# Optimization experiments

Hardware: AMD Instinct MI355X
Metric: run time of the kernel (lower is better)

Reference implementation:

```python
import jax, jax.numpy as jnp
import numpy as np

BATCH, SEQ = 4, 2048
D_MODEL, INNER, STATE, K, FFN = 384, 768, 16, 4, 1024


def setup_inputs() -> dict:
    key = jax.random.key(0)
    ks = jax.random.split(key, 12)
    def g(k, shape, scale=0.02):
        return jax.random.normal(k, shape, jnp.float32) * scale
    return {
        "x": jax.random.normal(ks[0], (BATCH, SEQ, D_MODEL), jnp.float32),
        "rms1_w": jnp.ones((D_MODEL,), jnp.float32),
        "rms2_w": jnp.ones((D_MODEL,), jnp.float32),
        "in_proj_w": g(ks[1], (D_MODEL, 2 * INNER)),
        "conv_w": g(ks[2], (K, INNER, INNER)),
        "conv_b": jnp.zeros((INNER,), jnp.float32),
        "x_proj_w": g(ks[3], (INNER, 2 * STATE)),
        "dt_proj_w": g(ks[4], (INNER, INNER)),
        "dt_proj_b": jnp.zeros((INNER,), jnp.float32),
        "A_log": jnp.log(jax.random.uniform(ks[5], (INNER, STATE), jnp.float32, 1.0, 16.0)),
        "D_param": jnp.ones((INNER,), jnp.float32),
        "out_proj_w": g(ks[6], (INNER, D_MODEL)),
        "ln_gamma": jnp.ones((D_MODEL,), jnp.float32),
        "ln_beta": jnp.zeros((D_MODEL,), jnp.float32),
        "gate_w": g(ks[7], (D_MODEL, FFN)),
        "up_w": g(ks[8], (D_MODEL, FFN)),
        "down_w": g(ks[9], (FFN, D_MODEL)),
    }


def rms_norm(x, w, eps=1e-6):
    norm = jnp.sqrt(jnp.mean(jnp.square(x), axis=-1, keepdims=True) + eps)
    return x / norm * w


def layer_norm(x, gamma, beta, eps=1e-5):
    mu = jnp.mean(x, axis=-1, keepdims=True)
    var = jnp.mean(jnp.square(x - mu), axis=-1, keepdims=True)
    return (x - mu) / jnp.sqrt(var + eps) * gamma + beta


def selective_scan(x, delta, A_log, Bm, Cm, Dp):
    # x, delta: [B,L,Di]; Bm, Cm: [B,L,N]; A_log: [Di,N]; Dp: [Di]
    delta = jax.nn.softplus(delta)
    A = -jnp.exp(A_log)                          # [Di,N]
    A_disc = jnp.exp(delta[..., None] * A)       # [B,L,Di,N]
    B_disc = delta[..., None] * Bm[:, :, None, :]  # [B,L,Di,N]
    xs = jnp.moveaxis(x, 1, 0)       # [L,B,Di]
    As = jnp.moveaxis(A_disc, 1, 0)  # [L,B,Di,N]
    Bs = jnp.moveaxis(B_disc, 1, 0)  # [L,B,Di,N]
    Cs = jnp.moveaxis(Cm, 1, 0)      # [L,B,N]
    h0 = jnp.zeros((x.shape[0], A_log.shape[0], A_log.shape[1]), x.dtype)
    def step(h, inp):
        x_t, A_t, B_t, C_t = inp
        h = A_t * h + B_t * x_t[..., None]          # [B,Di,N]
        y_t = jnp.einsum('bdn,bn->bd', h, C_t)      # [B,Di]
        return h, y_t
    _, ys = jax.lax.scan(step, h0, (xs, As, Bs, Cs))
    y = jnp.moveaxis(ys, 0, 1)       # [B,L,Di]
    return y + Dp * x


def mamba_core(h, in_proj_w, conv_w, conv_b, x_proj_w, dt_proj_w, dt_proj_b,
               A_log, D_param, out_proj_w, ln_gamma, ln_beta):
    xz = h @ in_proj_w                             # [B,L,2*Di]
    x_inner, z = jnp.split(xz, 2, axis=-1)
    # Conv1D SAME padding (k=4 -> pad (1,2)), channels-last, kernel [W,I,O]
    x_conv = jax.lax.conv_general_dilated(
        x_inner, conv_w, window_strides=(1,), padding='SAME',
        dimension_numbers=('NWC', 'WIO', 'NWC')) + conv_b
    x_conv = jax.nn.silu(x_conv)
    Bm, Cm = jnp.split(x_conv @ x_proj_w, 2, axis=-1)  # each [B,L,N]
    delta = x_conv @ dt_proj_w + dt_proj_b            # [B,L,Di]
    y = selective_scan(x_conv, delta, A_log, Bm, Cm, D_param)
    y = y * jax.nn.silu(z)
    out = y @ out_proj_w
    return layer_norm(out, ln_gamma, ln_beta)


def reference(x, rms1_w, rms2_w, in_proj_w, conv_w, conv_b, x_proj_w,
              dt_proj_w, dt_proj_b, A_log, D_param, out_proj_w, ln_gamma,
              ln_beta, gate_w, up_w, down_w):
    residual = x
    h = rms_norm(x, rms1_w)
    h = mamba_core(h, in_proj_w, conv_w, conv_b, x_proj_w, dt_proj_w,
                   dt_proj_b, A_log, D_param, out_proj_w, ln_gamma, ln_beta)
    x = residual + h  # dropout inactive (training=False)
    residual = x
    h = rms_norm(x, rms2_w)
    hidden = jax.nn.silu(h @ gate_w) * (h @ up_w)
    x = residual + hidden @ down_w
    return x
```

## Files before the change

kernel.cpp:

```cpp
#include <hip/hip_runtime.h>
#include <hip/hip_bf16.h>


using u16 = unsigned short;
using u32 = unsigned int;
using short8 = __attribute__((ext_vector_type(8))) short;
using f32x4  = __attribute__((ext_vector_type(4))) float;

#define TTOK 8192
#define DM 384
#define DI 768
#define NST 16
#define LSEQ 2048
#define NCH 64
#define LCH 32

#define SWZ_R(row, quad) \
  ((row) * 32 + ((((quad) ^ (row) ^ ((row) >> 2)) & 3) * 8))
#define SWZ_W(tid) SWZ_R((tid) >> 2, (tid) & 3)

__device__ __forceinline__ float bf2f(u16 a) {
  u32 u = ((u32)a) << 16;
  float f; __builtin_memcpy(&f, &u, 4); return f;
}
__device__ __forceinline__ u16 f2bf(float f) {
  u32 u; __builtin_memcpy(&u, &f, 4);
  u32 r = (u + 0x7fffu + ((u >> 16) & 1u)) >> 16;
  return (u16)r;
}
__device__ __forceinline__ int probe_bf(const void* rw) {
  return (((const u32*)rw)[0] == 0x3F803F80u) ? 1 : 0;
}
__device__ __forceinline__ float ld_in(const void* p, int i, int isbf) {
  return isbf ? bf2f(((const u16*)p)[i]) : ((const float*)p)[i];
}
__device__ __forceinline__ float fexp2(float x) {
#if __has_builtin(__builtin_amdgcn_exp2f)
  return __builtin_amdgcn_exp2f(x);
#else
  return exp2f(x);
#endif
}
__device__ __forceinline__ float wave_sum(float v) {
#pragma unroll
  for (int off = 32; off > 0; off >>= 1) v += __shfl_xor(v, off, 64);
  return v;
}

__device__ __forceinline__ void gl_lds16(const u16* g, u16* l) {
  __builtin_amdgcn_global_load_lds(
      (const __attribute__((address_space(1))) u32*)g,
      (__attribute__((address_space(3))) u32*)l, 16, 0, 0);
}

#define V_CB 0
#define V_DB 768
#define V_DP 1536
#define V_R1 2304
#define V_R2 2688
#define V_GA 3072
#define V_BE 3456

__global__ __launch_bounds__(256) void k_prep(
    const void* __restrict__ x, const void* __restrict__ in_proj,
    const void* __restrict__ conv_w, const void* __restrict__ dt_w,
    const void* __restrict__ x_proj, const void* __restrict__ out_proj,
    const void* __restrict__ gate_w, const void* __restrict__ up_w,
    const void* __restrict__ down_w, const void* __restrict__ A_log,
    const void* __restrict__ conv_b, const void* __restrict__ dt_b,
    const void* __restrict__ Dp, const void* __restrict__ rms1_w,
    const void* __restrict__ rms2_w, const void* __restrict__ gamma,
    const void* __restrict__ beta,
    u16* __restrict__ W1T, u16* __restrict__ WCT, u16* __restrict__ W45T,
    u16* __restrict__ W5T, u16* __restrict__ W6T, u16* __restrict__ W7T,
    float* __restrict__ An2T, u16* __restrict__ vecs,
    u16* __restrict__ WinX, u16* __restrict__ h1pad) {
  const int isbf = probe_bf(rms1_w);
  const int bx = blockIdx.x;
  const int tid = threadIdx.x;
  __shared__ u16 lt[64 * 66];

  if (bx < 1236) {
    const void* src; size_t soff = 0; u16* dst; int R, C, tpr, lo;
    if (bx < 144)       { src = in_proj;  dst = W1T;  R = 384;  C = 1536; tpr = 24; lo = bx; }
    else if (bx < 720)  { int tp = (bx - 144) / 144; lo = (bx - 144) % 144;
                          src = conv_w; soff = (size_t)tp * 589824;
                          dst = WCT + (size_t)tp * 589824; R = 768; C = 768; tpr = 12; }
    else if (bx < 864)  { src = dt_w;     dst = W45T; R = 768;  C = 768;  tpr = 12; lo = bx - 720; }
    else if (bx < 876)  { src = x_proj;   dst = W45T + (size_t)768 * 768;
                          R = 768; C = 32; tpr = 1; lo = bx - 864; }
    else if (bx < 948)  { src = out_proj; dst = W5T;  R = 768;  C = 384;  tpr = 6;  lo = bx - 876; }
    else if (bx < 1044) { src = gate_w;   dst = W6T;  R = 384;  C = 1024; tpr = 16; lo = bx - 948; }
    else if (bx < 1140) { src = up_w;     dst = W6T + (size_t)1024 * 384;
                          R = 384; C = 1024; tpr = 16; lo = bx - 1044; }
    else                { src = down_w;   dst = W7T;  R = 1024; C = 384;  tpr = 6;  lo = bx - 1140; }
    int tr = lo / tpr, tc = lo % tpr;
    int r0 = tr * 64, c0 = tc * 64;
#pragma unroll
    for (int i = 0; i < 16; ++i) {
      int el = i * 256 + tid, lr = el >> 6, lc = el & 63;
      if (c0 + lc < C)
        lt[lr * 66 + lc] =
            f2bf(ld_in(src, (int)(soff + (size_t)(r0 + lr) * C + c0 + lc), isbf));
    }
    __syncthreads();
#pragma unroll
    for (int i = 0; i < 16; ++i) {
      int el = i * 256 + tid, orow = el >> 6, oc = el & 63;
      if (c0 + orow < C)
        dst[(size_t)(c0 + orow) * R + r0 + oc] = lt[oc * 66 + orow];
    }
    return;
  }
  if (bx < 5332) {
    int half = tid >> 7;
    int t = (bx - 1236) * 2 + half;
    int tid2 = tid & 127;
    int lane = tid & 63, wv = tid >> 6;
    float v[3]; float q = 0.f;
#pragma unroll
    for (int j = 0; j < 3; ++j) {
      v[j] = ld_in(x, t * DM + tid2 + j * 128, isbf);
      q += v[j] * v[j];
    }
    q = wave_sum(q);
    float* rq = (float*)lt;
    if (lane == 0) rq[wv] = q;
    __syncthreads();
    float rr = rsqrtf((rq[half * 2] + rq[half * 2 + 1]) * (1.f / DM) + 1e-6f);
    int b = t >> 11, l = t & 2047;
    size_t orow = ((size_t)(b * 2051 + l + 1)) * DM;
#pragma unroll
    for (int j = 0; j < 3; ++j) {
      int i = tid2 + j * 128;
      h1pad[orow + i] = f2bf(v[j] * rr * ld_in(rms1_w, i, isbf));
    }
    return;
  }
  if (bx < 6484) {
    int lo = (bx - 5332) * 256 + tid;
    int i = lo / 768, j = lo % 768;
    WinX[lo] = f2bf(ld_in(in_proj, i * 1536 + j, isbf));
    return;
  }
  if (bx < 6532) {
    int lo = (bx - 6484) * 256 + tid;
    if (lo < 12288) {
      int d = lo >> 4, n = lo & 15;
      An2T[n * DI + d] = -__expf(ld_in(A_log, lo, isbf)) * 1.44269504f;
    }
    return;
  }
  if (bx < 6547) {
    int lo = (bx - 6532) * 256 + tid;
    if (lo < 3840) {
      const void* s; int o;
      if      (lo < 768)  { s = conv_b; o = lo; }
      else if (lo < 1536) { s = dt_b;   o = lo - 768; }
      else if (lo < 2304) { s = Dp;     o = lo - 1536; }
      else if (lo < 2688) { s = rms1_w; o = lo - 2304; }
      else if (lo < 3072) { s = rms2_w; o = lo - 2688; }
      else if (lo < 3456) { s = gamma;  o = lo - 3072; }
      else                { s = beta;   o = lo - 3456; }
      vecs[lo] = f2bf(ld_in(s, o, isbf));
    }
    return;
  }
  {
    int lo = (bx - 6547) * 256 + tid;
    if (lo < 4608) {
      int b = lo / (3 * DM), rem = lo % (3 * DM);
      int which = rem / DM, i = rem % DM;
      int row = b * 2051 + (which == 0 ? 0 : (2048 + which));
      h1pad[(size_t)row * DM + i] = 0;
    }
  }
}

__global__ __launch_bounds__(128) void k_lnrms(const float* __restrict__ outm,
                                               const void* __restrict__ xin,
                                               const void* __restrict__ rw,
                                               const u16* __restrict__ vecs,
                                               float* __restrict__ x2f,
                                               u16* __restrict__ h2) {
  const int isbf = probe_bf(rw);
  int t = blockIdx.x, tid = threadIdx.x;
  int lane = tid & 63, wid = tid >> 6;
  float v[3]; float s = 0.f, q = 0.f;
#pragma unroll
  for (int j = 0; j < 3; ++j) {
    v[j] = outm[(size_t)t * DM + tid + j * 128];
    s += v[j]; q += v[j] * v[j];
  }
  s = wave_sum(s); q = wave_sum(q);
  __shared__ float rs[2], rq[2], r2[2];
  if (lane == 0) { rs[wid] = s; rq[wid] = q; }
  __syncthreads();
  float mu = (rs[0] + rs[1]) * (1.f / DM);
  float var = (rq[0] + rq[1]) * (1.f / DM) - mu * mu;
  float rstd = rsqrtf(var + 1e-5f);
  float x2v[3]; float q2 = 0.f;
#pragma unroll
  for (int j = 0; j < 3; ++j) {
    int i = tid + j * 128;
    float ln = (v[j] - mu) * rstd * bf2f(vecs[V_GA + i]) + bf2f(vecs[V_BE + i]);
    x2v[j] = ld_in(xin, t * DM + i, isbf) + ln;
    x2f[(size_t)t * DM + i] = x2v[j];
    q2 += x2v[j] * x2v[j];
  }
  q2 = wave_sum(q2);
  if (lane == 0) r2[wid] = q2;
  __syncthreads();
  float rr = rsqrtf((r2[0] + r2[1]) * (1.f / DM) + 1e-6f);
#pragma unroll
  for (int j = 0; j < 3; ++j) {
    int i = tid + j * 128;
    h2[(size_t)t * DM + i] = f2bf(x2v[j] * rr * bf2f(vecs[V_R2 + i]));
  }
}

template <int EPI, int KDIM>
__global__ __launch_bounds__(256) void gemm_bt(
    const u16* __restrict__ A, const u16* __restrict__ BT,
    float* __restrict__ o1, u16* __restrict__ ob1,
    const float* __restrict__ res, const void* __restrict__ fl) {
  __shared__ u16 smem[2][8192];
  const int tid = threadIdx.x;
  const int lane = tid & 63, wid = tid >> 6;
  const int wm = (wid >> 1) << 5, wn = (wid & 1) << 5;
  const int fr = lane & 15, quad = lane >> 4;
  const int m0 = blockIdx.x * 64, n0 = blockIdx.y * 64;

  f32x4 acc[2][2] = {};

  const int wrow = (wid << 4) | (lane >> 2);
  const int sq = ((lane & 3) ^ wrow ^ (wrow >> 2)) & 3;
  const u16* BTe = (EPI == 6) ? BT + (size_t)blockIdx.z * 589824 : BT;
  const u16* srcA = A + (size_t)(m0 + wrow) * KDIM + sq * 8;
  const u16* srcB = BTe + (size_t)(n0 + wrow) * KDIM + sq * 8;
  u16* lw = &smem[0][0] + (wid << 9);

  auto stage = [&](int buf, int kt) {
    u16* lb = lw + buf * 8192;
    gl_lds16(srcA + kt,      lb);
    gl_lds16(srcA + kt + 32, lb + 2048);
    gl_lds16(srcB + kt,      lb + 4096);
    gl_lds16(srcB + kt + 32, lb + 6144);
  };

  stage(0, 0);
  int cur = 0;

#pragma unroll 1
  for (int kt = 0; kt < KDIM; kt += 64) {
    __syncthreads();
    if (kt + 64 < KDIM) stage(cur ^ 1, kt + 64);
    const u16* sm = &smem[cur][0];
#pragma unroll
    for (int kh = 0; kh < 2; ++kh) {
      const int ao = kh * 2048, bo = 4096 + kh * 2048;
      short8 af[2], bfg[2];
#pragma unroll
      for (int i = 0; i < 2; ++i)
        af[i] = *(const short8*)&sm[ao + SWZ_R(wm + i * 16 + fr, quad)];
#pragma unroll
      for (int i = 0; i < 2; ++i)
        bfg[i] = *(const short8*)&sm[bo + SWZ_R(wn + i * 16 + fr, quad)];
#pragma unroll
      for (int mt = 0; mt < 2; ++mt)
#pragma unroll
        for (int nt = 0; nt < 2; ++nt)
          acc[mt][nt] = __builtin_amdgcn_mfma_f32_16x16x32_bf16(
              af[mt], bfg[nt], acc[mt][nt], 0, 0, 0);
    }
    cur ^= 1;
  }

  int isbf = 0;
  if (EPI == 5) isbf = probe_bf(fl);

#pragma unroll
  for (int mt = 0; mt < 2; ++mt) {
#pragma unroll
    for (int nt = 0; nt < 2; ++nt) {
#pragma unroll
      for (int r = 0; r < 4; ++r) {
        int t = m0 + wm + mt * 16 + quad * 4 + r;
        int n = n0 + wn + nt * 16 + fr;
        float v = acc[mt][nt][r];
        if (EPI == 3) {
          o1[(size_t)t * DM + n] = v;
        } else if (EPI == 5) {
          float val = v + res[(size_t)t * DM + n];
          if (isbf) ob1[(size_t)t * DM + n] = f2bf(val);
          else      o1[(size_t)t * DM + n] = val;
        } else if (EPI == 6) {
          ob1[(size_t)n * 1536 + blockIdx.z * 384 + t] = f2bf(v);
        }
      }
    }
  }
}

__global__ __launch_bounds__(256) void gemm2_128(
    const u16* __restrict__ A, const u16* __restrict__ BT,
    float* __restrict__ o2, u16* __restrict__ ob1,
    const u16* __restrict__ bias) {
  constexpr int KDIM = 768;
  __shared__ u16 smem[2][12288];
  const int tid = threadIdx.x;
  const int lane = tid & 63, wid = tid >> 6;
  const int wm = (wid >> 1) << 6, wn = (wid & 1) << 5;
  const int fr = lane & 15, quad = lane >> 4;
  const int m0 = blockIdx.x * 128, n0 = blockIdx.y * 64;

  f32x4 acc[4][2] = {};

  const int ra = (wid << 5) | (lane >> 2);
  const int sqa = ((lane & 3) ^ ra ^ (ra >> 2)) & 3;
  const int rb = (wid << 4) | (lane >> 2);
  const int sqb = ((lane & 3) ^ rb ^ (rb >> 2)) & 3;
  const u16* srcA = A + (size_t)(m0 + ra) * KDIM + sqa * 8;
  const u16* srcB = BT + (size_t)(n0 + rb) * KDIM + sqb * 8;
  u16* lA = &smem[0][0] + (wid << 10);
  u16* lB = &smem[0][8192] + (wid << 9);

  auto stage = [&](int buf, int kt) {
    u16* a = lA + buf * 12288;
    u16* b = lB + buf * 12288;
    gl_lds16(srcA + kt,                           a);
    gl_lds16(srcA + kt + (size_t)16 * KDIM,       a + 512);
    gl_lds16(srcA + kt + 32,                      a + 4096);
    gl_lds16(srcA + kt + 32 + (size_t)16 * KDIM,  a + 4608);
    gl_lds16(srcB + kt,       b);
    gl_lds16(srcB + kt + 32,  b + 2048);
  };

  stage(0, 0);
  int cur = 0;

#pragma unroll 1
  for (int kt = 0; kt < KDIM; kt += 64) {
    __syncthreads();
    if (kt + 64 < KDIM) stage(cur ^ 1, kt + 64);
    const u16* sm = &smem[cur][0];
#pragma unroll
    for (int kh = 0; kh < 2; ++kh) {
      const int ao = kh * 4096, bo = 8192 + kh * 2048;
      short8 af[4], bfg[2];
#pragma unroll
      for (int i = 0; i < 4; ++i)
        af[i] = *(const short8*)&sm[ao + SWZ_R(wm + i * 16 + fr, quad)];
#pragma unroll
      for (int i = 0; i < 2; ++i)
        bfg[i] = *(const short8*)&sm[bo + SWZ_R(wn + i * 16 + fr, quad)];
#pragma unroll
      for (int mt = 0; mt < 4; ++mt)
#pragma unroll
        for (int nt = 0; nt < 2; ++nt)
          acc[mt][nt] = __builtin_amdgcn_mfma_f32_16x16x32_bf16(
              af[mt], bfg[nt], acc[mt][nt], 0, 0, 0);
    }
    cur ^= 1;
  }

#pragma unroll
  for (int nt = 0; nt < 2; ++nt) {
    const int n = n0 + wn + nt * 16 + fr;
    if (n < DI) {
      const float bv = bf2f(bias[n]);
#pragma unroll
      for (int mt = 0; mt < 4; ++mt) {
#pragma unroll
        for (int r = 0; r < 4; ++r) {
          int t = m0 + wm + mt * 16 + quad * 4 + r;
          float xx = acc[mt][nt][r] + bv;
          float e = fexp2(xx * 1.44269504f);
          float sp = (xx > 20.f) ? xx : 0.69314718056f * __log2f(1.f + e);
          ob1[(size_t)t * DI + n] = f2bf(sp);
        }
      }
    } else if (n < DI + 32) {
#pragma unroll
      for (int mt = 0; mt < 4; ++mt) {
#pragma unroll
        for (int r = 0; r < 4; ++r) {
          int t = m0 + wm + mt * 16 + quad * 4 + r;
          o2[(size_t)t * 32 + (n - DI)] = acc[mt][nt][r];
        }
      }
    }
  }
}

__global__ __launch_bounds__(256) void gemm_xz(
    const u16* __restrict__ A, const u16* __restrict__ WC,
    const u16* __restrict__ WZ, u16* __restrict__ xconv,
    u16* __restrict__ zbuf, const u16* __restrict__ bias) {
  __shared__ u16 smem[12288];
  const int tid = threadIdx.x;
  const int lane = tid & 63, wid = tid >> 6;
  const int wm = (wid >> 1) << 6, wn = (wid & 1) << 5;
  const int fr = lane & 15, quad = lane >> 4;
  const int yb = blockIdx.y;
  const bool isz = yb >= 12;
  const int kd = isz ? 384 : 1536;
  const u16* BT = isz ? WZ : WC;
  const int kldb = isz ? 384 : 1536;
  const int n0 = (isz ? yb - 12 : yb) * 64;
  const int m0 = blockIdx.x * 128;

  f32x4 acc[4][2] = {};

  const int ra = (wid << 5) | (lane >> 2);
  const int sqa = ((lane & 3) ^ ra ^ (ra >> 2)) & 3;
  const int rb = (wid << 4) | (lane >> 2);
  const int sqb = ((lane & 3) ^ rb ^ (rb >> 2)) & 3;
  const u16* srcB = BT + (size_t)(n0 + rb) * kldb + sqb * 8;
  const int b = m0 >> 11, l0 = m0 & 2047;
  const u16* srcA0 =
      A + (size_t)(b * 2051 + l0 + ra + (isz ? 1 : 0)) * DM + sqa * 8;
  u16* lA = &smem[0] + (wid << 10);
  u16* lB = &smem[8192] + (wid << 9);

  int wc = 0, ic = 0;
  auto stage = [&](int kt) {
    const u16* sa = srcA0 + (size_t)wc * DM + ic;
    gl_lds16(sa,                         lA);
    gl_lds16(sa + (size_t)16 * DM,       lA + 512);
    gl_lds16(sa + 32,                    lA + 4096);
    gl_lds16(sa + 32 + (size_t)16 * DM,  lA + 4608);
    gl_lds16(srcB + kt,       lB);
    gl_lds16(srcB + kt + 32,  lB + 2048);
    ic += 64; if (ic == 384) { ic = 0; ++wc; }
  };

#pragma unroll 1
  for (int kt = 0; kt < kd; kt += 64) {
    __syncthreads();
    stage(kt);
    __syncthreads();
#pragma unroll
    for (int kh = 0; kh < 2; ++kh) {
      const int ao = kh * 4096, bo = 8192 + kh * 2048;
      short8 af[4], bfg[2];
#pragma unroll
      for (int i = 0; i < 4; ++i)
        af[i] = *(const short8*)&smem[ao + SWZ_R(wm + i * 16 + fr, quad)];
#pragma unroll
      for (int i = 0; i < 2; ++i)
        bfg[i] = *(const short8*)&smem[bo + SWZ_R(wn + i * 16 + fr, quad)];
#pragma unroll
      for (int mt = 0; mt < 4; ++mt)
#pragma unroll
        for (int nt = 0; nt < 2; ++nt)
          acc[mt][nt] = __builtin_amdgcn_mfma_f32_16x16x32_bf16(
              af[mt], bfg[nt], acc[mt][nt], 0, 0, 0);
    }
  }

#pragma unroll
  for (int mt = 0; mt < 4; ++mt) {
#pragma unroll
    for (int nt = 0; nt < 2; ++nt) {
#pragma unroll
      for (int r = 0; r < 4; ++r) {
        int t = m0 + wm + mt * 16 + quad * 4 + r;
        int n = n0 + wn + nt * 16 + fr;
        float v = acc[mt][nt][r];
        if (isz) {
          zbuf[(size_t)t * DI + n] = f2bf(v);
        } else {
          float xx = v + bf2f(bias[n]);
          float sg = 1.f / (1.f + __expf(-xx));
          xconv[(size_t)t * DI + n] = f2bf(xx * sg);
        }
      }
    }
  }
}

__global__ __launch_bounds__(256) void gemm_gu(
    const u16* __restrict__ A, const u16* __restrict__ W6T,
    u16* __restrict__ hid) {
  __shared__ u16 smem[16384];
  const int tid = threadIdx.x;
  const int lane = tid & 63, wid = tid >> 6;
  const int wm = (wid >> 1) << 6, wn = (wid & 1) << 5;
  const int fr = lane & 15, quad = lane >> 4;
  const int m0 = blockIdx.x * 128, n0 = blockIdx.y * 64;

  f32x4 accg[4][2] = {}, accu[4][2] = {};

  const int ra = (wid << 5) | (lane >> 2);
  const int sqa = ((lane & 3) ^ ra ^ (ra >> 2)) & 3;
  const int rb = (wid << 4) | (lane >> 2);
  const int sqb = ((lane & 3) ^ rb ^ (rb >> 2)) & 3;
  const u16* srcA = A + (size_t)(m0 + ra) * DM + sqa * 8;
  const u16* srcG = W6T + (size_t)(n0 + rb) * DM + sqb * 8;
  const u16* srcU = W6T + (size_t)(1024 + n0 + rb) * DM + sqb * 8;
  u16* lA = &smem[0] + (wid << 10);
  u16* lG = &smem[8192] + (wid << 9);
  u16* lU = &smem[12288] + (wid << 9);

  auto stage = [&](int kt) {
    gl_lds16(srcA + kt,                        lA);
    gl_lds16(srcA + kt + (size_t)16 * DM,      lA + 512);
    gl_lds16(srcA + kt + 32,                   lA + 4096);
    gl_lds16(srcA + kt + 32 + (size_t)16 * DM, lA + 4608);
    gl_lds16(srcG + kt,       lG);
    gl_lds16(srcG + kt + 32,  lG + 2048);
    gl_lds16(srcU + kt,       lU);
    gl_lds16(srcU + kt + 32,  lU + 2048);
  };

#pragma unroll 1
  for (int kt = 0; kt < DM; kt += 64) {
    __syncthreads();
    stage(kt);
    __syncthreads();
#pragma unroll
    for (int kh = 0; kh < 2; ++kh) {
      const int ao = kh * 4096, go = 8192 + kh * 2048, uo = 12288 + kh * 2048;
      short8 af[4], bg[2], bu[2];
#pragma unroll
      for (int i = 0; i < 4; ++i)
        af[i] = *(const short8*)&smem[ao + SWZ_R(wm + i * 16 + fr, quad)];
#pragma unroll
      for (int i = 0; i < 2; ++i) {
        bg[i] = *(const short8*)&smem[go + SWZ_R(wn + i * 16 + fr, quad)];
        bu[i] = *(const short8*)&smem[uo + SWZ_R(wn + i * 16 + fr, quad)];
      }
#pragma unroll
      for (int mt = 0; mt < 4; ++mt)
#pragma unroll
        for (int nt = 0; nt < 2; ++nt) {
          accg[mt][nt] = __builtin_amdgcn_mfma_f32_16x16x32_bf16(
              af[mt], bg[nt], accg[mt][nt], 0, 0, 0);
          accu[mt][nt] = __builtin_amdgcn_mfma_f32_16x16x32_bf16(
              af[mt], bu[nt], accu[mt][nt], 0, 0, 0);
        }
    }
  }

#pragma unroll
  for (int mt = 0; mt < 4; ++mt) {
#pragma unroll
    for (int nt = 0; nt < 2; ++nt) {
#pragma unroll
      for (int r = 0; r < 4; ++r) {
        int t = m0 + wm + mt * 16 + quad * 4 + r;
        int n = n0 + wn + nt * 16 + fr;
        float g = accg[mt][nt][r];
        float u = accu[mt][nt][r];
        float sg = 1.f / (1.f + __expf(-g));
        hid[(size_t)t * 1024 + n] = f2bf(g * sg * u);
      }
    }
  }
}

__global__ __launch_bounds__(256) void k_scan1(
    const u16* __restrict__ deltab, const u16* __restrict__ xconv,
    const float* __restrict__ BC, const float* __restrict__ An2T,
    float* __restrict__ hlb, float* __restrict__ Pb) {
  __shared__ float bcs[LCH * 32];
  int gid = blockIdx.x * 256 + threadIdx.x;
  int d = gid % DI, bc = gid / DI, c = bc & (NCH - 1), b = bc >> 6;
  int row0 = b * LSEQ + c * LCH;
  ((float4*)bcs)[threadIdx.x] =
      ((const float4*)(BC + (size_t)row0 * 32))[threadIdx.x];
  float An[NST];
#pragma unroll
  for (int n = 0; n < NST; ++n) An[n] = An2T[n * DI + d];
  float h[NST], P[NST];
#pragma unroll
  for (int n = 0; n < NST; ++n) { h[n] = 0.f; P[n] = 1.f; }
  float dt = bf2f(deltab[(size_t)row0 * DI + d]);
  float xv = bf2f(xconv[(size_t)row0 * DI + d]);
  __syncthreads();
  for (int s = 0; s < LCH; ++s) {
    float dtc = dt, xvc = xv;
    if (s + 1 < LCH) {
      int r2 = row0 + s + 1;
      dt = bf2f(deltab[(size_t)r2 * DI + d]);
      xv = bf2f(xconv[(size_t)r2 * DI + d]);
    }
    const float4* br = (const float4*)&bcs[s * 32];
    float4 q0 = br[0], q1 = br[1], q2 = br[2], q3 = br[3];
    float Bm[NST] = {q0.x, q0.y, q0.z, q0.w, q1.x, q1.y, q1.z, q1.w,
                     q2.x, q2.y, q2.z, q2.w, q3.x, q3.y, q3.z, q3.w};
    float dxv = dtc * xvc;
#pragma unroll
    for (int n = 0; n < NST; ++n) {
      float a = fexp2(dtc * An[n]);
      h[n] = fmaf(a, h[n], dxv * Bm[n]);
      P[n] *= a;
    }
  }
  float4* ph = (float4*)(hlb + (size_t)gid * NST);
  float4* pp = (float4*)(Pb + (size_t)gid * NST);
#pragma unroll
  for (int i = 0; i < 4; ++i) {
    ph[i] = make_float4(h[4*i], h[4*i+1], h[4*i+2], h[4*i+3]);
    pp[i] = make_float4(P[4*i], P[4*i+1], P[4*i+2], P[4*i+3]);
  }
}

__global__ __launch_bounds__(256) void k_scan2(const float* __restrict__ hlb,
                                               const float* __restrict__ Pb,
                                               float* __restrict__ hin) {
  int gid = blockIdx.x * 256 + threadIdx.x;
  int n = gid & 15, bd = gid >> 4;
  int d = bd % DI, b = bd / DI;
  size_t base = ((size_t)(b * NCH) * DI + d) * NST + n;
  const size_t cstride = (size_t)DI * NST;
  float H = 0.f;
  float hc = hlb[base], pc = Pb[base];
  for (int c = 0; c < NCH; ++c) {
    size_t idx = base + (size_t)c * cstride;
    float hn = 0.f, pn = 0.f;
    if (c + 1 < NCH) { hn = hlb[idx + cstride]; pn = Pb[idx + cstride]; }
    hin[idx] = H;
    H = hc + pc * H;
    hc = hn; pc = pn;
  }
}

__global__ __launch_bounds__(256) void k_scan3(
    const u16* __restrict__ deltab, const u16* __restrict__ xconv,
    const float* __restrict__ BC, const float* __restrict__ An2T,
    const float* __restrict__ hinb, const u16* __restrict__ zb,
    const u16* __restrict__ vecs, u16* __restrict__ ys) {
  __shared__ float bcs[LCH * 32];
  int gid = blockIdx.x * 256 + threadIdx.x;
  int d = gid % DI, bc = gid / DI, c = bc & (NCH - 1), b = bc >> 6;
  int row0 = b * LSEQ + c * LCH;
  ((float4*)bcs)[threadIdx.x] =
      ((const float4*)(BC + (size_t)row0 * 32))[threadIdx.x];
  float An[NST];
#pragma unroll
  for (int n = 0; n < NST; ++n) An[n] = An2T[n * DI + d];
  float h[NST];
  {
    const float4* hp = (const float4*)(hinb + (size_t)gid * NST);
#pragma unroll
    for (int i = 0; i < 4; ++i) {
      float4 t = hp[i];
      h[4*i] = t.x; h[4*i+1] = t.y; h[4*i+2] = t.z; h[4*i+3] = t.w;
    }
  }
  float Dd = bf2f(vecs[V_DP + d]);
  float dt = bf2f(deltab[(size_t)row0 * DI + d]);
  float xv = bf2f(xconv[(size_t)row0 * DI + d]);
  float zv = bf2f(zb[(size_t)row0 * DI + d]);
  __syncthreads();
  for (int s = 0; s < LCH; ++s) {
    int row = row0 + s;
    float dtc = dt, xvc = xv, zvc = zv;
    if (s + 1 < LCH) {
      int r2 = row + 1;
      dt = bf2f(deltab[(size_t)r2 * DI + d]);
      xv = bf2f(xconv[(size_t)r2 * DI + d]);
      zv = bf2f(zb[(size_t)r2 * DI + d]);
    }
    const float4* br = (const float4*)&bcs[s * 32];
    float4 q0 = br[0], q1 = br[1], q2 = br[2], q3 = br[3];
    float4 c0 = br[4], c1 = br[5], c2 = br[6], c3 = br[7];
    float Bm[NST] = {q0.x, q0.y, q0.z, q0.w, q1.x, q1.y, q1.z, q1.w,
                     q2.x, q2.y, q2.z, q2.w, q3.x, q3.y, q3.z, q3.w};
    float Cm[NST] = {c0.x, c0.y, c0.z, c0.w, c1.x, c1.y, c1.z, c1.w,
                     c2.x, c2.y, c2.z, c2.w, c3.x, c3.y, c3.z, c3.w};
    float dxv = dtc * xvc;
    float yp[4] = {0.f, 0.f, 0.f, 0.f};
#pragma unroll
    for (int n = 0; n < NST; ++n) {
      float a = fexp2(dtc * An[n]);
      h[n] = fmaf(a, h[n], dxv * Bm[n]);
      yp[n & 3] = fmaf(h[n], Cm[n], yp[n & 3]);
    }
    float y = (yp[0] + yp[1]) + (yp[2] + yp[3]);
    float sz = zvc / (1.f + __expf(-zvc));
    ys[(size_t)row * DI + d] = f2bf((y + Dd * xvc) * sz);
  }
}

extern "C" void kernel_launch(void* const* d_in, const int* in_sizes, int n_in,
                              void* d_out, int out_size, void* d_ws,
                              size_t ws_size, hipStream_t stream) {
  (void)in_sizes; (void)n_in; (void)out_size;
  const void* x        = d_in[0];
  const void* rms1_w   = d_in[1];
  const void* rms2_w   = d_in[2];
  const void* in_proj  = d_in[3];
  const void* conv_w   = d_in[4];
  const void* conv_b   = d_in[5];
  const void* x_proj   = d_in[6];
  const void* dt_w     = d_in[7];
  const void* dt_b     = d_in[8];
  const void* A_log    = d_in[9];
  const void* Dp       = d_in[10];
  const void* out_proj = d_in[11];
  const void* gamma    = d_in[12];
  const void* beta     = d_in[13];
  const void* gate_w   = d_in[14];
  const void* up_w     = d_in[15];
  const void* down_w   = d_in[16];

  char* ws = (char*)d_ws;
  size_t off = 0;
  auto alloc = [&](size_t bytes) -> void* {
    void* p = ws + off;
    off = (off + bytes + 255) & ~(size_t)255;
    return p;
  };
  u16*   W1T   = (u16*)alloc((size_t)1536 * 384 * 2);
  u16*   WCT   = (u16*)alloc((size_t)4 * 768 * 768 * 2);
  u16*   W45T  = (u16*)alloc((size_t)896 * 768 * 2);
  u16*   W5T   = (u16*)alloc((size_t)384 * 768 * 2);
  u16*   W6T   = (u16*)alloc((size_t)2048 * 384 * 2);
  u16*   W7T   = (u16*)alloc((size_t)384 * 1024 * 2);
  float* An2T  = (float*)alloc((size_t)16 * 768 * 4);
  u16*   vecs  = (u16*)alloc(3840 * 2);
  u16*   WinX  = (u16*)alloc((size_t)384 * 768 * 2);
  u16*   WcombT= (u16*)alloc((size_t)768 * 1536 * 2);
  u16*   h1pad = (u16*)alloc((size_t)4 * 2051 * 384 * 2);
  u16*   zbuf  = (u16*)alloc((size_t)8192 * 768 * 2);
  u16*   xconv = (u16*)alloc((size_t)8192 * 768 * 2);
  u16*   deltab= (u16*)alloc((size_t)8192 * 768 * 2);
  float* BCb   = (float*)alloc((size_t)8192 * 32 * 4);
  float* hl    = (float*)alloc((size_t)196608 * 16 * 4);
  float* Pb    = (float*)alloc((size_t)196608 * 16 * 4);
  float* hin   = (float*)alloc((size_t)196608 * 16 * 4);
  u16*   ys   = (u16*)hl;
  float* outm = Pb;
  float* x2f  = hin;
  u16*   h2   = h1pad;
  u16*   hid  = (u16*)hl;

  if (off > ws_size) return;

  k_prep<<<6565, 256, 0, stream>>>(
      x, in_proj, conv_w, dt_w, x_proj, out_proj, gate_w, up_w, down_w,
      A_log, conv_b, dt_b, Dp, rms1_w, rms2_w, gamma, beta,
      W1T, WCT, W45T, W5T, W6T, W7T, An2T, vecs, WinX, h1pad);

  gemm_bt<6, 768><<<dim3(6, 12, 4), 256, 0, stream>>>(
      WinX, WCT, nullptr, WcombT, nullptr, nullptr);

  gemm_xz<<<dim3(64, 24), 256, 0, stream>>>(
      h1pad, WcombT, W1T + (size_t)768 * 384, xconv, zbuf, vecs + V_CB);

  gemm2_128<<<dim3(64, 13), 256, 0, stream>>>(
      xconv, W45T, BCb, deltab, vecs + V_DB);

  k_scan1<<<768, 256, 0, stream>>>(deltab, xconv, BCb, An2T, hl, Pb);
  k_scan2<<<192, 256, 0, stream>>>(hl, Pb, hin);
  k_scan3<<<768, 256, 0, stream>>>(deltab, xconv, BCb, An2T, hin, zbuf, vecs,
                                   ys);

  gemm_bt<3, 768><<<dim3(128, 6), 256, 0, stream>>>(
      ys, W5T, outm, nullptr, nullptr, nullptr);
  k_lnrms<<<8192, 128, 0, stream>>>(outm, x, rms1_w, vecs, x2f, h2);

  gemm_gu<<<dim3(64, 16), 256, 0, stream>>>(h2, W6T, hid);
  gemm_bt<5, 1024><<<dim3(128, 6), 256, 0, stream>>>(
      hid, W7T, (float*)d_out, (u16*)d_out, x2f, rms1_w);
}
```

Measured before the change: 305.4 us.

## Double-buffer gemm_xz LDS and replace per-state chunk decay products with delta sums

gemm_xz now uses two LDS buffers and prefetches the next k-tile while computing the current one, which removes one barrier per iteration. This mirrors the gemm_bt pipeline and doubles the kernel's shared memory. The chunked scan no longer accumulates and stores a per-state decay product P. Scan1 stores only the sum of delta per chunk and channel, and scan2 rebuilds P as exp2(An*S), which cuts the writes and reads of a large float buffer at the cost of one exp per step. The rebuilt P can differ slightly in rounding from the old running product.

```diff
diff --git a/kernel.cpp b/kernel.cpp
--- a/kernel.cpp
+++ b/kernel.cpp
@@ -327,13 +327,13 @@
 
   auto stage = [&](int buf, int kt) {
     u16* a = lA + buf * 12288;
-    u16* b = lB + buf * 12288;
+    u16* bb = lB + buf * 12288;
     gl_lds16(srcA + kt,                           a);
     gl_lds16(srcA + kt + (size_t)16 * KDIM,       a + 512);
     gl_lds16(srcA + kt + 32,                      a + 4096);
     gl_lds16(srcA + kt + 32 + (size_t)16 * KDIM,  a + 4608);
-    gl_lds16(srcB + kt,       b);
-    gl_lds16(srcB + kt + 32,  b + 2048);
+    gl_lds16(srcB + kt,       bb);
+    gl_lds16(srcB + kt + 32,  bb + 2048);
   };
 
   stage(0, 0);
@@ -397,7 +397,7 @@
     const u16* __restrict__ A, const u16* __restrict__ WC,
     const u16* __restrict__ WZ, u16* __restrict__ xconv,
     u16* __restrict__ zbuf, const u16* __restrict__ bias) {
-  __shared__ u16 smem[12288];
+  __shared__ u16 smem[2][12288];
   const int tid = threadIdx.x;
   const int lane = tid & 63, wid = tid >> 6;
   const int wm = (wid >> 1) << 6, wn = (wid & 1) << 5;
@@ -420,36 +420,41 @@
   const int b = m0 >> 11, l0 = m0 & 2047;
   const u16* srcA0 =
       A + (size_t)(b * 2051 + l0 + ra + (isz ? 1 : 0)) * DM + sqa * 8;
-  u16* lA = &smem[0] + (wid << 10);
-  u16* lB = &smem[8192] + (wid << 9);
+  u16* lA = &smem[0][0] + (wid << 10);
+  u16* lB = &smem[0][8192] + (wid << 9);
 
   int wc = 0, ic = 0;
-  auto stage = [&](int kt) {
+  auto stage = [&](int buf, int kt) {
     const u16* sa = srcA0 + (size_t)wc * DM + ic;
-    gl_lds16(sa,                         lA);
-    gl_lds16(sa + (size_t)16 * DM,       lA + 512);
-    gl_lds16(sa + 32,                    lA + 4096);
-    gl_lds16(sa + 32 + (size_t)16 * DM,  lA + 4608);
-    gl_lds16(srcB + kt,       lB);
-    gl_lds16(srcB + kt + 32,  lB + 2048);
+    u16* a = lA + buf * 12288;
+    u16* bb = lB + buf * 12288;
+    gl_lds16(sa,                         a);
+    gl_lds16(sa + (size_t)16 * DM,       a + 512);
+    gl_lds16(sa + 32,                    a + 4096);
+    gl_lds16(sa + 32 + (size_t)16 * DM,  a + 4608);
+    gl_lds16(srcB + kt,       bb);
+    gl_lds16(srcB + kt + 32,  bb + 2048);
     ic += 64; if (ic == 384) { ic = 0; ++wc; }
   };
+
+  stage(0, 0);
+  int cur = 0;
 
 #pragma unroll 1
   for (int kt = 0; kt < kd; kt += 64) {
     __syncthreads();
-    stage(kt);
-    __syncthreads();
+    if (kt + 64 < kd) stage(cur ^ 1, kt + 64);
+    const u16* sm = &smem[cur][0];
 #pragma unroll
     for (int kh = 0; kh < 2; ++kh) {
       const int ao = kh * 4096, bo = 8192 + kh * 2048;
       short8 af[4], bfg[2];
 #pragma unroll
       for (int i = 0; i < 4; ++i)
-        af[i] = *(const short8*)&smem[ao + SWZ_R(wm + i * 16 + fr, quad)];
+        af[i] = *(const short8*)&sm[ao + SWZ_R(wm + i * 16 + fr, quad)];
 #pragma unroll
       for (int i = 0; i < 2; ++i)
-        bfg[i] = *(const short8*)&smem[bo + SWZ_R(wn + i * 16 + fr, quad)];
+        bfg[i] = *(const short8*)&sm[bo + SWZ_R(wn + i * 16 + fr, quad)];
 #pragma unroll
       for (int mt = 0; mt < 4; ++mt)
 #pragma unroll
@@ -457,6 +462,7 @@
           acc[mt][nt] = __builtin_amdgcn_mfma_f32_16x16x32_bf16(
               af[mt], bfg[nt], acc[mt][nt], 0, 0, 0);
     }
+    cur ^= 1;
   }
 
 #pragma unroll
@@ -563,7 +569,7 @@
 __global__ __launch_bounds__(256) void k_scan1(
     const u16* __restrict__ deltab, const u16* __restrict__ xconv,
     const float* __restrict__ BC, const float* __restrict__ An2T,
-    float* __restrict__ hlb, float* __restrict__ Pb) {
+    float* __restrict__ hlb, float* __restrict__ Sb) {
   __shared__ float bcs[LCH * 32];
   int gid = blockIdx.x * 256 + threadIdx.x;
   int d = gid % DI, bc = gid / DI, c = bc & (NCH - 1), b = bc >> 6;
@@ -573,9 +579,10 @@
   float An[NST];
 #pragma unroll
   for (int n = 0; n < NST; ++n) An[n] = An2T[n * DI + d];
-  float h[NST], P[NST];
-#pragma unroll
-  for (int n = 0; n < NST; ++n) { h[n] = 0.f; P[n] = 1.f; }
+  float h[NST];
+#pragma unroll
+  for (int n = 0; n < NST; ++n) h[n] = 0.f;
+  float S = 0.f;
   float dt = bf2f(deltab[(size_t)row0 * DI + d]);
   float xv = bf2f(xconv[(size_t)row0 * DI + d]);
   __syncthreads();
@@ -591,39 +598,37 @@
     float Bm[NST] = {q0.x, q0.y, q0.z, q0.w, q1.x, q1.y, q1.z, q1.w,
                      q2.x, q2.y, q2.z, q2.w, q3.x, q3.y, q3.z, q3.w};
     float dxv = dtc * xvc;
+    S += dtc;
 #pragma unroll
     for (int n = 0; n < NST; ++n) {
       float a = fexp2(dtc * An[n]);
       h[n] = fmaf(a, h[n], dxv * Bm[n]);
-      P[n] *= a;
     }
   }
   float4* ph = (float4*)(hlb + (size_t)gid * NST);
-  float4* pp = (float4*)(Pb + (size_t)gid * NST);
-#pragma unroll
-  for (int i = 0; i < 4; ++i) {
+#pragma unroll
+  for (int i = 0; i < 4; ++i)
     ph[i] = make_float4(h[4*i], h[4*i+1], h[4*i+2], h[4*i+3]);
-    pp[i] = make_float4(P[4*i], P[4*i+1], P[4*i+2], P[4*i+3]);
-  }
+  Sb[gid] = S;
 }
 
 __global__ __launch_bounds__(256) void k_scan2(const float* __restrict__ hlb,
-                                               const float* __restrict__ Pb,
+                                               const float* __restrict__ Sb,
+                                               const float* __restrict__ An2T,
                                                float* __restrict__ hin) {
   int gid = blockIdx.x * 256 + threadIdx.x;
   int n = gid & 15, bd = gid >> 4;
   int d = bd % DI, b = bd / DI;
+  float An = An2T[n * DI + d];
   size_t base = ((size_t)(b * NCH) * DI + d) * NST + n;
+  size_t sbase = (size_t)(b * NCH) * DI + d;
   const size_t cstride = (size_t)DI * NST;
   float H = 0.f;
-  float hc = hlb[base], pc = Pb[base];
   for (int c = 0; c < NCH; ++c) {
     size_t idx = base + (size_t)c * cstride;
-    float hn = 0.f, pn = 0.f;
-    if (c + 1 < NCH) { hn = hlb[idx + cstride]; pn = Pb[idx + cstride]; }
+    float P = fexp2(An * Sb[sbase + (size_t)c * DI]);
     hin[idx] = H;
-    H = hc + pc * H;
-    hc = hn; pc = pn;
+    H = hlb[idx] + P * H;
   }
 }
 
@@ -732,6 +737,7 @@
   float* hl    = (float*)alloc((size_t)196608 * 16 * 4);
   float* Pb    = (float*)alloc((size_t)196608 * 16 * 4);
   float* hin   = (float*)alloc((size_t)196608 * 16 * 4);
+  float* Sb    = (float*)alloc((size_t)196608 * 4);
   u16*   ys   = (u16*)hl;
   float* outm = Pb;
   float* x2f  = hin;
@@ -754,8 +760,8 @@
   gemm2_128<<<dim3(64, 13), 256, 0, stream>>>(
       xconv, W45T, BCb, deltab, vecs + V_DB);
 
-  k_scan1<<<768, 256, 0, stream>>>(deltab, xconv, BCb, An2T, hl, Pb);
-  k_scan2<<<192, 256, 0, stream>>>(hl, Pb, hin);
+  k_scan1<<<768, 256, 0, stream>>>(deltab, xconv, BCb, An2T, hl, Sb);
+  k_scan2<<<192, 256, 0, stream>>>(hl, Sb, An2T, hin);
   k_scan3<<<768, 256, 0, stream>>>(deltab, xconv, BCb, An2T, hin, zbuf, vecs,
                                    ys);
 
```

After: 308.5 us. No clear change (+1.0%).
